# Kernel optimization log

Measured on AMD Instinct MI355X. Metric: run time of the kernel, lower is better.

The kernel has to match this reference:

```python
import jax, jax.numpy as jnp
import numpy as np

B, N, K, D, V, L = 16, 512, 16, 256, 64, 2


def setup_inputs() -> dict:
    key = jax.random.key(0)
    ks = jax.random.split(key, 20)
    inp = {
        "node_reps": jax.random.normal(ks[0], (B, N, D), dtype=jnp.float32),
        "mask": jax.random.uniform(ks[1], (B, N), dtype=jnp.float32),
        "in_indices": jax.random.randint(ks[2], (B, N, K), 0, N),
        "in_edges": jax.random.randint(ks[3], (B, N, K), 0, V),
        "in_mask": jax.random.uniform(ks[4], (B, N, K), dtype=jnp.float32),
        "out_indices": jax.random.randint(ks[5], (B, N, K), 0, N),
        "out_edges": jax.random.randint(ks[6], (B, N, K), 0, V),
        "out_mask": jax.random.uniform(ks[7], (B, N, K), dtype=jnp.float32),
        "edge_emb": jax.random.normal(ks[8], (V, D), dtype=jnp.float32) * 0.02,
        # packed gate weights, order [ig, fg, og, cell] along last dim
        "Wi": jax.random.normal(ks[9], (2 * D, 4 * D), dtype=jnp.float32) * 0.02,
        "Wo": jax.random.normal(ks[10], (2 * D, 4 * D), dtype=jnp.float32) * 0.02,
        "Ui": jax.random.normal(ks[11], (2 * D, 4 * D), dtype=jnp.float32) * 0.02,
        "Uo": jax.random.normal(ks[12], (2 * D, 4 * D), dtype=jnp.float32) * 0.02,
        "bi": jnp.zeros((4 * D,), dtype=jnp.float32),
        "bo": jnp.zeros((4 * D,), dtype=jnp.float32),
        "bui": jnp.zeros((4 * D,), dtype=jnp.float32),
        "buo": jnp.zeros((4 * D,), dtype=jnp.float32),
    }
    return inp


def _agg(h, idx, edge_reps, nmask):
    # gather neighbor states: [B,N,K,D]
    neigh = h[jnp.arange(h.shape[0])[:, None, None], idx]
    x = jnp.concatenate([neigh, edge_reps], axis=-1) * nmask[..., None]
    return x.sum(axis=2)  # [B,N,2D]


def reference(node_reps, mask, in_indices, in_edges, in_mask,
              out_indices, out_edges, out_mask,
              edge_emb, Wi, Wo, Ui, Uo, bi, bo, bui, buo):
    in_edge_reps = edge_emb[in_edges]    # [B,N,K,D]
    out_edge_reps = edge_emb[out_edges]  # [B,N,K,D]

    in_reps = _agg(node_reps, in_indices, in_edge_reps, in_mask)     # [B,N,2D]
    out_reps = _agg(node_reps, out_indices, out_edge_reps, out_mask)  # [B,N,2D]
    z_static = in_reps @ Wi + bi + out_reps @ Wo + bo  # [B,N,4D]

    h = node_reps
    c = jnp.zeros_like(node_reps)
    reps = []
    for _ in range(L):
        in_pre = _agg(h, in_indices, in_edge_reps, in_mask)
        out_pre = _agg(h, out_indices, out_edge_reps, out_mask)
        z = z_static + in_pre @ Ui + bui + out_pre @ Uo + buo  # [B,N,4D]
        ig, fg, og, ci = jnp.split(z, 4, axis=-1)
        ig = jax.nn.sigmoid(ig)
        fg = jax.nn.sigmoid(fg)
        og = jax.nn.sigmoid(og)
        ci = jnp.tanh(ci)
        c_new = fg * c + ig * ci
        h_new = og * jnp.tanh(c_new)
        c = c_new * mask[..., None]
        h = h_new * mask[..., None]
        reps.append(h)
    return (jnp.stack(reps, axis=0), h, c)
```

## Files before the change

### kernel.cpp

```cpp
#include <hip/hip_runtime.h>
#include <math.h>

#define Kn 16
#define Dd 256
#define NC 1024
#define XS 640
#define MR 8192

typedef _Float16 h8 __attribute__((ext_vector_type(8)));
typedef _Float16 h4 __attribute__((ext_vector_type(4)));
typedef _Float16 h2 __attribute__((ext_vector_type(2)));
typedef float f4 __attribute__((ext_vector_type(4)));

__device__ __forceinline__ void gload16(_Float16* lds, const _Float16* g) {
  __builtin_amdgcn_global_load_lds(
      (const __attribute__((address_space(1))) void*)g,
      (__attribute__((address_space(3))) void*)lds, 16, 0, 0);
}

__device__ __forceinline__ float fsigm(float x) { return 1.f / (1.f + __expf(-x)); }
__device__ __forceinline__ float ftanh(float x) { return 2.f / (1.f + __expf(-2.f * x)) - 1.f; }

__global__ __launch_bounds__(256, 4) void mega2_kernel(
    const float* __restrict__ node_reps, const float* __restrict__ emb,
    const int* __restrict__ iidx, const float* __restrict__ im,
    const int* __restrict__ oidx, const float* __restrict__ om,
    const int* __restrict__ ie, const int* __restrict__ oe,
    const float* __restrict__ Wi, const float* __restrict__ Wo,
    const float* __restrict__ Ui, const float* __restrict__ Uo,
    const float* __restrict__ bi, const float* __restrict__ bo,
    const float* __restrict__ bui, const float* __restrict__ buo,
    _Float16* __restrict__ X, _Float16* __restrict__ W0f,
    _Float16* __restrict__ Wlf, float* __restrict__ biasq) {
  __shared__ __align__(16) char smem[20480];
  const int b = blockIdx.x, t = threadIdx.x;

  if (b < 2048) {
    const int lane = t & 63;
    const int wid = t >> 6;
    const int row = (b & 7) * 1024 + (b >> 3) * 4 + wid;
    const int half = lane >> 5;
    const int lc = lane & 31;
    const int sel = lane >> 4, p16 = lane & 15;

    const int bb = row * Kn + p16;
    const int* ap = (sel == 0)   ? (iidx + bb)
                    : (sel == 1) ? ((const int*)im + bb)
                    : (sel == 2) ? (oidx + bb)
                                 : ((const int*)om + bb);
    const int cmb = *ap;
    const int cmbe = *(((lane & 16) ? oe : ie) + bb);

    const int hb = row & ~511;
    const float* hp = node_reps + ((size_t)hb << 8) + (lc << 3);

    float acc[8] = {};
#pragma unroll
    for (int kb = 0; kb < 2; kb++) {
      f4 w0[8], w1[8];
#pragma unroll
      for (int k = 0; k < 8; k++) {
        const int ik = __shfl(cmb, (lane & 32) | (kb * 8 + k), 64);
        const float* p = hp + ((size_t)ik << 8);
        w0[k] = *(const f4*)p;
        w1[k] = *(const f4*)(p + 4);
      }
      __builtin_amdgcn_sched_barrier(0);
#pragma unroll
      for (int k = 0; k < 8; k++) {
        const float mk = __int_as_float(__shfl(cmb, (lane & 32) | 16 | (kb * 8 + k), 64));
#pragma unroll
        for (int c = 0; c < 4; c++) {
          acc[c] += mk * w0[k][c];
          acc[4 + c] += mk * w1[k][c];
        }
      }
    }

    {
      float b0 = 0.f, b1 = 0.f;
      const int vmine = 2 * lane - half * 64;
#pragma unroll
      for (int k = 0; k < 16; k++) {
        const int ec = __shfl(cmbe, (half << 4) | k, 64);
        const float mc = __int_as_float(__shfl(cmb, (lane & 32) | 16 | k, 64));
        b0 += (ec == vmine) ? mc : 0.f;
        b1 += (ec == vmine + 1) ? mc : 0.f;
      }
      h2 bp;
      bp[0] = (_Float16)b0;
      bp[1] = (_Float16)b1;
      *(h2*)&X[(size_t)row * XS + 512 + lane * 2] = bp;
    }

    h8 o;
#pragma unroll
    for (int c = 0; c < 8; c++) o[c] = (_Float16)acc[c];
    *(h8*)&X[(size_t)row * XS + half * 256 + lc * 8] = o;
  } else if (b < 2176) {
    float* seT = (float*)smem;
    float* sa = (float*)(smem + 4096);
    const int pb = b - 2048;
    const int vgrp = pb >> 2, cq = pb & 3;
    const int dir = vgrp >> 4;
    const int v0 = (vgrp & 15) * 4;
    const float* Wa = dir ? Wo : Wi;
    const float* Ua = dir ? Uo : Ui;
#pragma unroll
    for (int r = 0; r < 4; r++) seT[t * 4 + r] = emb[(v0 + r) * 256 + t];
    __syncthreads();

    const int l = t & 63, ds = t >> 6;
    const int cp0 = cq * 256 + l * 4;
    const int g = (cp0 >> 4) & 3;
    const int d0 = ((cp0 >> 6) << 4) + (cp0 & 15);
    const int c0 = g * 256 + d0;
    const float* wp = Wa + (size_t)(256 + ds * 64) * NC + c0;
    const float* up = Ua + (size_t)(256 + ds * 64) * NC + c0;
    const float* sT = seT + (ds * 64) * 4;

    f4 av[4] = {};
    for (int bb8 = 0; bb8 < 8; bb8++) {
      f4 wv8[8], uv8[8];
#pragma unroll
      for (int ii = 0; ii < 8; ii++) {
        const int dd = bb8 * 8 + ii;
        wv8[ii] = *(const f4*)(wp + (size_t)dd * NC);
        uv8[ii] = *(const f4*)(up + (size_t)dd * NC);
      }
      __builtin_amdgcn_sched_barrier(0);
#pragma unroll
      for (int ii = 0; ii < 8; ii++) {
        const int dd = bb8 * 8 + ii;
        const f4 wv = wv8[ii] + uv8[ii];
        const f4 s0 = *(const f4*)&sT[dd * 4];
        av[0] += s0[0] * wv;
        av[1] += s0[1] * wv;
        av[2] += s0[2] * wv;
        av[3] += s0[3] * wv;
      }
    }
#pragma unroll
    for (int r = 0; r < 4; r++) *(f4*)&sa[((ds * 4 + r) * 64 + l) * 4] = av[r];
    __syncthreads();
    {
      const int r = t >> 6, fl = t & 63;
      f4 s = {0.f, 0.f, 0.f, 0.f};
#pragma unroll
      for (int d = 0; d < 4; d++) s += *(const f4*)&sa[((d * 4 + r) * 64 + fl) * 4];
      const int vvg = vgrp * 4 + r;
      const int kt = 16 + (vvg >> 5);
      const int lhi = (vvg >> 3) & 3;
      const int j = vvg & 7;
      const int cpb = cq * 256 + fl * 4;
#pragma unroll
      for (int i = 0; i < 4; i++) {
        const int cp = cpb + i;
        W0f[kt * 32768 + (cp >> 4) * 512 + (lhi * 16 + (cp & 15)) * 8 + j] = (_Float16)s[i];
      }
    }
  } else if (b < 2208) {
    const int p = b - 2176;
    const int kk = t >> 3;
    const int tc = t & 7;
    const int k = (p & 15) * 32 + kk;
    const float* rowp;
    const float* rowp2 = nullptr;
    if (p < 16) {
      rowp  = (k < 256) ? Wi + (size_t)k * NC : Wo + (size_t)(k - 256) * NC;
      rowp2 = (k < 256) ? Ui + (size_t)k * NC : Uo + (size_t)(k - 256) * NC;
    } else {
      rowp  = (k < 256) ? Ui + (size_t)k * NC : Uo + (size_t)(k - 256) * NC;
    }
    _Float16* dst = (p < 16) ? (W0f + p * 32768) : (Wlf + (p - 16) * 32768);
    const int lane0 = (kk >> 3) * 16;
    const int j = kk & 7;
    for (int bb8 = 0; bb8 < 4; bb8++) {
      f4 w8[8], u8[8];
#pragma unroll
      for (int ii = 0; ii < 8; ii++) {
        const int c = (bb8 * 8 + ii) * 32 + tc * 4;
        w8[ii] = *(const f4*)(rowp + c);
        if (p < 16) u8[ii] = *(const f4*)(rowp2 + c);
      }
      __builtin_amdgcn_sched_barrier(0);
#pragma unroll
      for (int ii = 0; ii < 8; ii++) {
        const int c = (bb8 * 8 + ii) * 32 + tc * 4;
        const int g = c >> 8, d = c & 255;
        const int nt = 4 * (d >> 4) + g;
        const int lb = lane0 + (d & 15);
        f4 v = w8[ii];
        if (p < 16) v += u8[ii];
#pragma unroll
        for (int q = 0; q < 4; q++)
          dst[nt * 512 + (lb + q) * 8 + j] = (_Float16)v[q];
      }
    }
  } else {
#pragma unroll
    for (int i = 0; i < 4; i++) {
      const int cq = t * 4 + i;
      const int dd = cq >> 2, g = cq & 3;
      const int c = g * 256 + dd;
      biasq[cq] = bi[c] + bo[c] + bui[c] + buo[c];
    }
  }
}

__global__ __launch_bounds__(256, 4) void agg_kernel(
    const _Float16* __restrict__ src,
    const int* __restrict__ iidx, const float* __restrict__ im,
    const int* __restrict__ oidx, const float* __restrict__ om,
    _Float16* __restrict__ X) {
  const int lane = threadIdx.x & 63;
  const int wid = threadIdx.x >> 6;
  const int b = blockIdx.x;
  const int row = (b & 7) * 1024 + (b >> 3) * 4 + wid;
  const int half = lane >> 5;
  const int lc = lane & 31;
  const int sel = lane >> 4, p16 = lane & 15;

  const int bb = row * Kn + p16;
  const int* ap = (sel == 0)   ? (iidx + bb)
                  : (sel == 1) ? ((const int*)im + bb)
                  : (sel == 2) ? (oidx + bb)
                               : ((const int*)om + bb);
  const int cmb = *ap;

  const int hb = row & ~511;
  const _Float16* hp = src + ((size_t)hb << 8) + (lc << 3);

  h8 w[16];
#pragma unroll
  for (int k = 0; k < 16; k++) {
    const int ik = __shfl(cmb, (lane & 32) | k, 64);
    w[k] = *(const h8*)(hp + ((size_t)ik << 8));
  }
  __builtin_amdgcn_sched_barrier(0);

  float acc[8] = {};
#pragma unroll
  for (int k = 0; k < 16; k++) {
    const float mk = __int_as_float(__shfl(cmb, (lane & 32) | 16 | k, 64));
#pragma unroll
    for (int c = 0; c < 8; c++) acc[c] += mk * (float)w[k][c];
  }

  h8 o;
#pragma unroll
  for (int c = 0; c < 8; c++) o[c] = (_Float16)acc[c];
  *(h8*)&X[(size_t)row * XS + half * 256 + lc * 8] = o;
}

template <bool WITH_Z>
__global__ __launch_bounds__(512) void fused_gemm(
    const _Float16* __restrict__ A, const _Float16* __restrict__ Wf,
    const float* __restrict__ biasq, _Float16* __restrict__ zq,
    const float* __restrict__ mask, const float* __restrict__ node_reps,
    float* __restrict__ reps, float* __restrict__ hbuf,
    _Float16* __restrict__ d16, float* __restrict__ cbuf) {
  constexpr int KT = WITH_Z ? 20 : 16;
  constexpr int D = 2;
  __shared__ __align__(16) _Float16 lds[3][8192];

  const int wg = (blockIdx.x & 7) * 64 + (blockIdx.x >> 3);
  const int bm = wg >> 3, bn = wg & 7;
  const int tid = threadIdx.x, lane = tid & 63, wid = tid >> 6;
  const int wr = wid >> 1, wc = wid & 1;
  const int lr = lane & 15, lg = lane >> 4;

  f4 acc[2][4] = {};

  const _Float16* srcA0 = A + (size_t)(bm * 128 + wid * 16 + lr) * XS + lg * 8;
  const _Float16* srcB0 = Wf + ((size_t)bn * 8 + wid) * 512 + lane * 8;
  const int woff = wid * 512;

  auto stage = [&](int buf, int kt) {
    _Float16* base = lds[buf];
    gload16(base + woff, srcA0 + kt * 32);
    gload16(base + 4096 + woff, srcB0 + (size_t)kt * 32768);
  };

  stage(0, 0);
  stage(1, 1);
  asm volatile("s_waitcnt vmcnt(%0)" :: "i"(D) : "memory");
  __builtin_amdgcn_s_barrier();

  int cur = 0;
  for (int kt = 0; kt < KT; kt++) {
    if (kt + 2 < KT) stage(cur == 0 ? 2 : cur - 1, kt + 2);

    const _Float16* base = lds[cur];
    h8 a[2], bfr[4];
#pragma unroll
    for (int m = 0; m < 2; m++) a[m] = *(const h8*)&base[(wr * 2 + m) * 512 + lane * 8];
#pragma unroll
    for (int n = 0; n < 4; n++) bfr[n] = *(const h8*)&base[4096 + (wc * 4 + n) * 512 + lane * 8];
    asm volatile("s_waitcnt lgkmcnt(0)" ::: "memory");
    __builtin_amdgcn_sched_barrier(0);

    __builtin_amdgcn_s_setprio(1);
#pragma unroll
    for (int m = 0; m < 2; m++)
#pragma unroll
      for (int n = 0; n < 4; n++)
        acc[m][n] = __builtin_amdgcn_mfma_f32_16x16x32_f16(a[m], bfr[n], acc[m][n], 0, 0, 0);
    __builtin_amdgcn_s_setprio(0);

    if (kt + 2 < KT) asm volatile("s_waitcnt vmcnt(%0)" :: "i"(D) : "memory");
    else             asm volatile("s_waitcnt vmcnt(0)" ::: "memory");
    __builtin_amdgcn_sched_barrier(0);
    __builtin_amdgcn_s_barrier();

    cur = (cur == 2) ? 0 : cur + 1;
  }

  const int d = (bn * 2 + wc) * 16 + lr;
  const int row0 = bm * 128 + wr * 32;
  f4 bq = {0.f, 0.f, 0.f, 0.f};
  if (WITH_Z) bq = *(const f4*)&biasq[d * 4];
#pragma unroll
  for (int i = 0; i < 2; i++) {
#pragma unroll
    for (int r = 0; r < 4; r++) {
      const int row = row0 + i * 16 + lg * 4 + r;
      const size_t off = (size_t)row * Dd + d;
      float zi, zf, zo, zc;
      if (WITH_Z) {
        zi = acc[i][0][r] + bq.x;
        zf = acc[i][1][r] + bq.y;
        zo = acc[i][2][r] + bq.z;
        zc = acc[i][3][r] + bq.w;
        h4 oz;
        oz[0] = (_Float16)zi; oz[1] = (_Float16)zf;
        oz[2] = (_Float16)zo; oz[3] = (_Float16)zc;
        *(h4*)&zq[off * 4] = oz;
      } else {
        const h4 zb = *(const h4*)&zq[off * 4];
        zi = (float)zb[0] + acc[i][0][r];
        zf = (float)zb[1] + acc[i][1][r];
        zo = (float)zb[2] + acc[i][2][r];
        zc = (float)zb[3] + acc[i][3][r];
      }
      const float ig = fsigm(zi), fg = fsigm(zf), og = fsigm(zo), ci = ftanh(zc);
      const float cold = WITH_Z ? 0.f : cbuf[off];
      const float cn = fg * cold + ig * ci;
      const float hn = og * ftanh(cn);
      const float mk = mask[row];
      cbuf[off] = cn * mk;
      const float hm = hn * mk;
      reps[off] = hm;
      if (WITH_Z) d16[off] = (_Float16)(hm - node_reps[off]);
      else        hbuf[off] = hm;
    }
  }
}

extern "C" void kernel_launch(void* const* d_in, const int* in_sizes, int n_in,
                              void* d_out, int out_size, void* d_ws, size_t ws_size,
                              hipStream_t stream) {
  const float* node_reps = (const float*)d_in[0];
  const float* mask      = (const float*)d_in[1];
  const int*   in_idx    = (const int*)d_in[2];
  const int*   in_edges  = (const int*)d_in[3];
  const float* in_mask   = (const float*)d_in[4];
  const int*   out_idx   = (const int*)d_in[5];
  const int*   out_edges = (const int*)d_in[6];
  const float* out_mask  = (const float*)d_in[7];
  const float* edge_emb  = (const float*)d_in[8];
  const float* Wi  = (const float*)d_in[9];
  const float* Wo  = (const float*)d_in[10];
  const float* Ui  = (const float*)d_in[11];
  const float* Uo  = (const float*)d_in[12];
  const float* bi  = (const float*)d_in[13];
  const float* bo  = (const float*)d_in[14];
  const float* bui = (const float*)d_in[15];
  const float* buo = (const float*)d_in[16];

  float* out = (float*)d_out;
  const size_t MD = (size_t)MR * Dd;
  float* reps0 = out;
  float* reps1 = out + MD;
  float* hbuf  = out + 2 * MD;
  float* cbuf  = out + 3 * MD;

  _Float16* X    = (_Float16*)d_ws;
  _Float16* zq   = X + (size_t)MR * XS;
  _Float16* W0f  = zq + (size_t)MR * NC;
  _Float16* Wlf  = W0f + 640 * 1024;
  _Float16* d16  = Wlf + 512 * 1024;
  float*    biasq = (float*)(d16 + (size_t)MR * Dd);

  mega2_kernel<<<2209, 256, 0, stream>>>(node_reps, edge_emb, in_idx, in_mask,
                                         out_idx, out_mask, in_edges, out_edges,
                                         Wi, Wo, Ui, Uo, bi, bo, bui, buo,
                                         X, W0f, Wlf, biasq);
  fused_gemm<true><<<512, 512, 0, stream>>>(
      X, W0f, biasq, zq, mask, node_reps, reps0, nullptr, d16, cbuf);
  agg_kernel<<<2048, 256, 0, stream>>>(d16, in_idx, in_mask, out_idx, out_mask, X);
  fused_gemm<false><<<512, 512, 0, stream>>>(
      X, Wlf, nullptr, zq, mask, nullptr, reps1, hbuf, nullptr, cbuf);
}
```

Measured before the change: 75.49 us.

## Recompute layer-0 cell state and store h instead of delta to cut traffic

The first fused GEMM no longer writes the cell state or reads node_reps. The second GEMM recomputes the old cell state from the stored fp16 z (sigmoid(zi)*tanh(zc)*mask). The aggregation kernel now gathers fp16 h and subtracts the previous X contents in its epilogue, which forms the delta, in place of gathering a precomputed h-node_reps difference. Final output stores use nontemporal hints. This removes several fp32 global reads and writes. The cost is an extra X read in the agg kernel and recomputed transcendentals, and cold is now derived from fp16-rounded z, which may change precision slightly.

```diff
diff --git a/kernel.cpp b/kernel.cpp
--- a/kernel.cpp
+++ b/kernel.cpp
@@ -230,6 +230,9 @@
 
   const int hb = row & ~511;
   const _Float16* hp = src + ((size_t)hb << 8) + (lc << 3);
+  _Float16* xp = &X[(size_t)row * XS + half * 256 + lc * 8];
+
+  const h8 xold = *(const h8*)xp;
 
   h8 w[16];
 #pragma unroll
@@ -249,17 +252,17 @@
 
   h8 o;
 #pragma unroll
-  for (int c = 0; c < 8; c++) o[c] = (_Float16)acc[c];
-  *(h8*)&X[(size_t)row * XS + half * 256 + lc * 8] = o;
+  for (int c = 0; c < 8; c++) o[c] = (_Float16)(acc[c] - (float)xold[c]);
+  *(h8*)xp = o;
 }
 
 template <bool WITH_Z>
 __global__ __launch_bounds__(512) void fused_gemm(
     const _Float16* __restrict__ A, const _Float16* __restrict__ Wf,
     const float* __restrict__ biasq, _Float16* __restrict__ zq,
-    const float* __restrict__ mask, const float* __restrict__ node_reps,
+    const float* __restrict__ mask,
     float* __restrict__ reps, float* __restrict__ hbuf,
-    _Float16* __restrict__ d16, float* __restrict__ cbuf) {
+    _Float16* __restrict__ h16, float* __restrict__ cbuf) {
   constexpr int KT = WITH_Z ? 20 : 16;
   constexpr int D = 2;
   __shared__ __align__(16) _Float16 lds[3][8192];
@@ -326,7 +329,8 @@
     for (int r = 0; r < 4; r++) {
       const int row = row0 + i * 16 + lg * 4 + r;
       const size_t off = (size_t)row * Dd + d;
-      float zi, zf, zo, zc;
+      const float mk = mask[row];
+      float zi, zf, zo, zc, cold;
       if (WITH_Z) {
         zi = acc[i][0][r] + bq.x;
         zf = acc[i][1][r] + bq.y;
@@ -336,23 +340,27 @@
         oz[0] = (_Float16)zi; oz[1] = (_Float16)zf;
         oz[2] = (_Float16)zo; oz[3] = (_Float16)zc;
         *(h4*)&zq[off * 4] = oz;
+        cold = 0.f;
       } else {
         const h4 zb = *(const h4*)&zq[off * 4];
         zi = (float)zb[0] + acc[i][0][r];
         zf = (float)zb[1] + acc[i][1][r];
         zo = (float)zb[2] + acc[i][2][r];
         zc = (float)zb[3] + acc[i][3][r];
+        cold = fsigm((float)zb[0]) * ftanh((float)zb[3]) * mk;
       }
       const float ig = fsigm(zi), fg = fsigm(zf), og = fsigm(zo), ci = ftanh(zc);
-      const float cold = WITH_Z ? 0.f : cbuf[off];
       const float cn = fg * cold + ig * ci;
       const float hn = og * ftanh(cn);
-      const float mk = mask[row];
-      cbuf[off] = cn * mk;
       const float hm = hn * mk;
-      reps[off] = hm;
-      if (WITH_Z) d16[off] = (_Float16)(hm - node_reps[off]);
-      else        hbuf[off] = hm;
+      if (WITH_Z) {
+        __builtin_nontemporal_store(hm, &reps[off]);
+        h16[off] = (_Float16)hm;
+      } else {
+        __builtin_nontemporal_store(hm, &reps[off]);
+        __builtin_nontemporal_store(hm, &hbuf[off]);
+        __builtin_nontemporal_store(cn * mk, &cbuf[off]);
+      }
     }
   }
 }
@@ -389,16 +397,16 @@
   _Float16* zq   = X + (size_t)MR * XS;
   _Float16* W0f  = zq + (size_t)MR * NC;
   _Float16* Wlf  = W0f + 640 * 1024;
-  _Float16* d16  = Wlf + 512 * 1024;
-  float*    biasq = (float*)(d16 + (size_t)MR * Dd);
+  _Float16* h16  = Wlf + 512 * 1024;
+  float*    biasq = (float*)(h16 + (size_t)MR * Dd);
 
   mega2_kernel<<<2209, 256, 0, stream>>>(node_reps, edge_emb, in_idx, in_mask,
                                          out_idx, out_mask, in_edges, out_edges,
                                          Wi, Wo, Ui, Uo, bi, bo, bui, buo,
                                          X, W0f, Wlf, biasq);
   fused_gemm<true><<<512, 512, 0, stream>>>(
-      X, W0f, biasq, zq, mask, node_reps, reps0, nullptr, d16, cbuf);
-  agg_kernel<<<2048, 256, 0, stream>>>(d16, in_idx, in_mask, out_idx, out_mask, X);
+      X, W0f, biasq, zq, mask, reps0, nullptr, h16, nullptr);
+  agg_kernel<<<2048, 256, 0, stream>>>(h16, in_idx, in_mask, out_idx, out_mask, X);
   fused_gemm<false><<<512, 512, 0, stream>>>(
-      X, Wlf, nullptr, zq, mask, nullptr, reps1, hbuf, nullptr, cbuf);
+      X, Wlf, nullptr, zq, mask, reps1, hbuf, nullptr, cbuf);
 }
```

Measured after the change: 72.20 us. 1.05x faster.
